# Kernel optimization log

Measured on AMD Instinct MI355X. Metric: run time of the kernel, lower is better.

## Reference

```python
import jax, jax.numpy as jnp
import numpy as np
from jax import lax

T = 64
TAU = 2.0
ALPHA = 4.0  # spikingjelly surrogate.Sigmoid default
V_TH = 1.0

@jax.custom_vjp
def spike(v):
    # Heaviside(v) with sigmoid surrogate gradient
    return (v >= 0.0).astype(v.dtype)

def _spike_fwd(v):
    return spike(v), v

def _spike_bwd(v, g):
    s = jax.nn.sigmoid(ALPHA * v)
    return (g * ALPHA * s * (1.0 - s),)

spike.defvjp(_spike_fwd, _spike_bwd)

def setup_inputs() -> dict:
    key = jax.random.key(0)
    k1, k2, k3 = jax.random.split(key, 3)
    x = jax.random.normal(k1, (2048, 28, 28), dtype=jnp.float32)
    W1 = jax.random.normal(k2, (1024, 784), dtype=jnp.float32) * (1.0 / np.sqrt(784))
    W2 = jax.random.normal(k3, (10, 1024), dtype=jnp.float32) * (1.0 / np.sqrt(1024))
    return {"x": x, "W1": W1, "W2": W2}

def _lif_step(v, c):
    # decay_input=True: v += (x - (v - v_reset)) / tau, v_reset = 0
    v = v + (c - v) / TAU
    s = spike(v - V_TH)
    v = v * (1.0 - s)  # hard reset to 0
    return v, s

def reference(x, W1, W2):
    B = x.shape[0]
    xf = x.reshape(B, -1)                      # [B, 784]
    c1 = xf @ W1.T                              # [B, 1024], identical every timestep
    v1_0 = jnp.zeros((B, W1.shape[0]), x.dtype)
    v2_0 = jnp.zeros((B, W2.shape[0]), x.dtype)

    def step(carry, _):
        v1, v2 = carry
        v1, s1 = _lif_step(v1, c1)              # [B, 1024]
        c2 = s1 @ W2.T                          # [B, 10]
        v2, s2 = _lif_step(v2, c2)              # [B, 10]
        return (v1, v2), s2

    _, out = lax.scan(step, (v1_0, v2_0), None, length=T)
    return out  # [T, B, 10]
```

## Files before the change

### kernel.cpp

```cpp
#include <hip/hip_runtime.h>
#include <stdint.h>

typedef unsigned long long u64;
typedef unsigned int u32;

#define T_STEPS 64
#define KDIM 784
#define N1 1024
#define NB 2048
#define N2 10

__global__ void k_w2t(const float* __restrict__ W2, float* __restrict__ W2T) {
    int j = blockIdx.x * blockDim.x + threadIdx.x;
    if (j >= N1) return;
    float r[12];
#pragma unroll
    for (int i = 0; i < 10; ++i) r[i] = W2[i * N1 + j];
    r[10] = 0.f; r[11] = 0.f;
#pragma unroll
    for (int i = 0; i < 12; ++i) W2T[j * 12 + i] = r[i];
}

#define BM 64
#define BN 64
#define BK 16

__global__ __launch_bounds__(256) void k_gemm_lif1(
    const float* __restrict__ X, const float* __restrict__ W1,
    u64* __restrict__ bits)
{
    __shared__ __align__(16) float As[BK][BM];
    __shared__ __align__(16) float Bs[BK][BN];

    const int tid = threadIdx.x;
    const int tx = tid & 15;
    const int ty = tid >> 4;
    const int bm = blockIdx.y * BM;
    const int bn = blockIdx.x * BN;

    const int lrow = tid >> 2;
    const int lk   = (tid & 3) << 2;

    const float* xa = X  + (size_t)(bm + lrow) * KDIM + lk;
    const float* wa = W1 + (size_t)(bn + lrow) * KDIM + lk;

    float acc[4][4];
#pragma unroll
    for (int r = 0; r < 4; ++r)
#pragma unroll
        for (int c = 0; c < 4; ++c) acc[r][c] = 0.f;

    float4 a = *(const float4*)(xa);
    float4 b = *(const float4*)(wa);

    for (int k0 = 0; k0 < KDIM; k0 += BK) {
        __syncthreads();
        As[lk+0][lrow] = a.x; As[lk+1][lrow] = a.y; As[lk+2][lrow] = a.z; As[lk+3][lrow] = a.w;
        Bs[lk+0][lrow] = b.x; Bs[lk+1][lrow] = b.y; Bs[lk+2][lrow] = b.z; Bs[lk+3][lrow] = b.w;
        __syncthreads();
        if (k0 + BK < KDIM) {
            a = *(const float4*)(xa + k0 + BK);
            b = *(const float4*)(wa + k0 + BK);
        }
#pragma unroll
        for (int kk = 0; kk < BK; ++kk) {
            float4 av = *(const float4*)(&As[kk][ty << 2]);
            float4 bv = *(const float4*)(&Bs[kk][tx << 2]);
            acc[0][0] += av.x * bv.x; acc[0][1] += av.x * bv.y; acc[0][2] += av.x * bv.z; acc[0][3] += av.x * bv.w;
            acc[1][0] += av.y * bv.x; acc[1][1] += av.y * bv.y; acc[1][2] += av.y * bv.z; acc[1][3] += av.y * bv.w;
            acc[2][0] += av.z * bv.x; acc[2][1] += av.z * bv.y; acc[2][2] += av.z * bv.z; acc[2][3] += av.z * bv.w;
            acc[3][0] += av.w * bv.x; acc[3][1] += av.w * bv.y; acc[3][2] += av.w * bv.z; acc[3][3] += av.w * bv.w;
        }
    }

    float c[16], v[16];
    u32 blo[16], bhi[16];
#pragma unroll
    for (int u = 0; u < 16; ++u) {
        c[u] = acc[u >> 2][u & 3];
        v[u] = 0.f; blo[u] = 0u; bhi[u] = 0u;
    }
    for (int t = 0; t < 32; ++t) {
#pragma unroll
        for (int u = 0; u < 16; ++u) {
            v[u] += (c[u] - v[u]) * 0.5f;
            bool s = v[u] >= 1.0f;
            blo[u] |= (s ? 1u : 0u) << t;
            v[u] = s ? 0.f : v[u];
        }
    }
    for (int t = 0; t < 32; ++t) {
#pragma unroll
        for (int u = 0; u < 16; ++u) {
            v[u] += (c[u] - v[u]) * 0.5f;
            bool s = v[u] >= 1.0f;
            bhi[u] |= (s ? 1u : 0u) << t;
            v[u] = s ? 0.f : v[u];
        }
    }
#pragma unroll
    for (int u = 0; u < 16; ++u) {
        int r = u >> 2, cc = u & 3;
        bits[(size_t)(bm + (ty << 2) + r) * N1 + (bn + (tx << 2) + cc)] =
            ((u64)bhi[u] << 32) | (u64)blo[u];
    }
}

__global__ __launch_bounds__(256) void k_lif2(
    const u64* __restrict__ bits, const float* __restrict__ W2T,
    float* __restrict__ out)
{
    __shared__ u64  masksS[4][N1];
    __shared__ u32  idxS[4][N1];
    __shared__ float c2S[4][64][12];
    __shared__ float s2S[4][64][10];

    const int tid  = threadIdx.x;
    const int w    = tid >> 6;
    const int lane = tid & 63;
    const int b    = (blockIdx.x << 2) + w;

    const u64* row = bits + (size_t)b * N1;

    int nact = 0;
#pragma unroll
    for (int it = 0; it < 16; ++it) {
        u64 m = row[lane + (it << 6)];
        u64 ball = __ballot(m != 0ULL);
        int pos = nact + __popcll(ball & ((1ULL << lane) - 1ULL));
        if (m != 0ULL) { masksS[w][pos] = m; idxS[w][pos] = lane + (it << 6); }
        nact += __popcll(ball);
    }

    float acc[10];
#pragma unroll
    for (int i = 0; i < 10; ++i) acc[i] = 0.f;

#define LIF2_BODY(A)                                                      \
    {                                                                     \
        u64 m = masksS[w][(A)];                                           \
        int j = __builtin_amdgcn_readfirstlane((int)idxS[w][(A)]);        \
        float sf = (float)((m >> lane) & 1ULL);                           \
        const float* wr = W2T + j * 12;                                   \
        float4 w0 = *(const float4*)(wr);                                 \
        float4 w1 = *(const float4*)(wr + 4);                             \
        float2 w2 = *(const float2*)(wr + 8);                             \
        acc[0] += sf * w0.x; acc[1] += sf * w0.y;                         \
        acc[2] += sf * w0.z; acc[3] += sf * w0.w;                         \
        acc[4] += sf * w1.x; acc[5] += sf * w1.y;                         \
        acc[6] += sf * w1.z; acc[7] += sf * w1.w;                         \
        acc[8] += sf * w2.x; acc[9] += sf * w2.y;                         \
    }

    int a = 0;
    for (; a + 2 <= nact; a += 2) { LIF2_BODY(a); LIF2_BODY(a + 1); }
    if (a < nact) LIF2_BODY(a);
#undef LIF2_BODY

#pragma unroll
    for (int i = 0; i < 10; ++i) c2S[w][lane][i] = acc[i];
    __syncthreads();

    if (tid < 40) {
        const int w2 = tid / 10, i = tid % 10;
        float v2 = 0.f;
        for (int t = 0; t < 64; ++t) {
            float cc = c2S[w2][t][i];
            v2 += (cc - v2) * 0.5f;
            bool s = v2 >= 1.0f;
            s2S[w2][t][i] = s ? 1.f : 0.f;
            v2 = s ? 0.f : v2;
        }
    }
    __syncthreads();

    const int b0 = blockIdx.x << 2;
    for (int idx = tid; idx < 64 * 40; idx += 256) {
        int t = idx / 40, r = idx % 40;
        out[(size_t)t * (NB * N2) + (size_t)b0 * N2 + r] = s2S[r / 10][t][r % 10];
    }
}

extern "C" void kernel_launch(void* const* d_in, const int* in_sizes, int n_in,
                              void* d_out, int out_size, void* d_ws, size_t ws_size,
                              hipStream_t stream) {
    const float* X  = (const float*)d_in[0];
    const float* W1 = (const float*)d_in[1];
    const float* W2 = (const float*)d_in[2];
    float* out = (float*)d_out;

    u64*   bits = (u64*)d_ws;
    float* W2T  = (float*)((char*)d_ws + (size_t)NB * N1 * sizeof(u64));

    k_w2t<<<dim3((N1 + 255) / 256), dim3(256), 0, stream>>>(W2, W2T);

    dim3 g1(N1 / BN, NB / BM);
    k_gemm_lif1<<<g1, dim3(256), 0, stream>>>(X, W1, bits);

    k_lif2<<<dim3(NB / 4), dim3(256), 0, stream>>>(bits, W2T, out);
}
```

Before: 166.1 us.

## Transpose X and W1 to K-major and compute GEMM without shared memory

Adds a kernel that transposes X and W1 into K-major layouts in workspace. The GEMM+LIF1 kernel is rewritten so each lane owns one output neuron and loops over K, reading W1t coalesced per lane and a wave-uniform 16-row slice of Xt as broadcast float4 loads, with no LDS tiling or barriers. The goal is to remove shared-memory staging and synchronisation overhead. In exchange it adds an extra transpose pass over about 9.5 MB of data and relies on scalar/broadcast loads plus the cache for reuse, with only 16 outputs per thread.

```diff
diff --git a/kernel.cpp b/kernel.cpp
--- a/kernel.cpp
+++ b/kernel.cpp
@@ -21,69 +21,79 @@
     for (int i = 0; i < 12; ++i) W2T[j * 12 + i] = r[i];
 }
 
-#define BM 64
-#define BN 64
-#define BK 16
+__global__ __launch_bounds__(256) void k_transpose2(
+    const float* __restrict__ X, float* __restrict__ Xt,
+    const float* __restrict__ W1, float* __restrict__ W1t)
+{
+    __shared__ float t[32][33];
+    int b = blockIdx.x;
+    const float* src; float* dst; int R;
+    int tile_r, tile_c;
+    if (b < 1600) { src = X;  dst = Xt;  R = NB; tile_r = b / 25; tile_c = b % 25; }
+    else { b -= 1600; src = W1; dst = W1t; R = N1; tile_r = b / 25; tile_c = b % 25; }
+
+    const int tx = threadIdx.x & 31, ty = threadIdx.x >> 5;
+    const int r0 = tile_r << 5, c0 = tile_c << 5;
+
+#pragma unroll
+    for (int i = 0; i < 32; i += 8) {
+        int c = c0 + tx;
+        t[ty + i][tx] = (c < KDIM) ? src[(size_t)(r0 + ty + i) * KDIM + c] : 0.f;
+    }
+    __syncthreads();
+#pragma unroll
+    for (int i = 0; i < 32; i += 8) {
+        int c = c0 + ty + i;
+        if (c < KDIM) dst[(size_t)c * R + r0 + tx] = t[tx][ty + i];
+    }
+}
 
 __global__ __launch_bounds__(256) void k_gemm_lif1(
-    const float* __restrict__ X, const float* __restrict__ W1,
+    const float* __restrict__ Xt,
+    const float* __restrict__ W1t,
     u64* __restrict__ bits)
 {
-    __shared__ __align__(16) float As[BK][BM];
-    __shared__ __align__(16) float Bs[BK][BN];
-
-    const int tid = threadIdx.x;
-    const int tx = tid & 15;
-    const int ty = tid >> 4;
-    const int bm = blockIdx.y * BM;
-    const int bn = blockIdx.x * BN;
-
-    const int lrow = tid >> 2;
-    const int lk   = (tid & 3) << 2;
-
-    const float* xa = X  + (size_t)(bm + lrow) * KDIM + lk;
-    const float* wa = W1 + (size_t)(bn + lrow) * KDIM + lk;
-
-    float acc[4][4];
-#pragma unroll
-    for (int r = 0; r < 4; ++r)
-#pragma unroll
-        for (int c = 0; c < 4; ++c) acc[r][c] = 0.f;
-
-    float4 a = *(const float4*)(xa);
-    float4 b = *(const float4*)(wa);
-
-    for (int k0 = 0; k0 < KDIM; k0 += BK) {
-        __syncthreads();
-        As[lk+0][lrow] = a.x; As[lk+1][lrow] = a.y; As[lk+2][lrow] = a.z; As[lk+3][lrow] = a.w;
-        Bs[lk+0][lrow] = b.x; Bs[lk+1][lrow] = b.y; Bs[lk+2][lrow] = b.z; Bs[lk+3][lrow] = b.w;
-        __syncthreads();
-        if (k0 + BK < KDIM) {
-            a = *(const float4*)(xa + k0 + BK);
-            b = *(const float4*)(wa + k0 + BK);
-        }
-#pragma unroll
-        for (int kk = 0; kk < BK; ++kk) {
-            float4 av = *(const float4*)(&As[kk][ty << 2]);
-            float4 bv = *(const float4*)(&Bs[kk][tx << 2]);
-            acc[0][0] += av.x * bv.x; acc[0][1] += av.x * bv.y; acc[0][2] += av.x * bv.z; acc[0][3] += av.x * bv.w;
-            acc[1][0] += av.y * bv.x; acc[1][1] += av.y * bv.y; acc[1][2] += av.y * bv.z; acc[1][3] += av.y * bv.w;
-            acc[2][0] += av.z * bv.x; acc[2][1] += av.z * bv.y; acc[2][2] += av.z * bv.z; acc[2][3] += av.z * bv.w;
-            acc[3][0] += av.w * bv.x; acc[3][1] += av.w * bv.y; acc[3][2] += av.w * bv.z; acc[3][3] += av.w * bv.w;
-        }
-    }
-
-    float c[16], v[16];
+    const int tid  = threadIdx.x;
+    const int wv   = tid >> 6;
+    const int lane = tid & 63;
+    const int bx   = blockIdx.x;
+
+    const int n0 = (bx & 15) << 6;
+    const int m0 = __builtin_amdgcn_readfirstlane(((bx >> 4) << 6) + (wv << 4));
+
+    const int n = n0 + lane;
+    const float*  __restrict__ wrow = W1t + n;
+    const float4* __restrict__ xrow = (const float4*)(Xt + m0);
+
+    float acc[16];
+#pragma unroll
+    for (int i = 0; i < 16; ++i) acc[i] = 0.f;
+
+#pragma unroll 4
+    for (int k = 0; k < KDIM; ++k) {
+        float a  = wrow[(size_t)k * N1];
+        float4 x0 = xrow[(size_t)k * 512 + 0];
+        float4 x1 = xrow[(size_t)k * 512 + 1];
+        float4 x2 = xrow[(size_t)k * 512 + 2];
+        float4 x3 = xrow[(size_t)k * 512 + 3];
+        acc[ 0] = fmaf(a, x0.x, acc[ 0]); acc[ 1] = fmaf(a, x0.y, acc[ 1]);
+        acc[ 2] = fmaf(a, x0.z, acc[ 2]); acc[ 3] = fmaf(a, x0.w, acc[ 3]);
+        acc[ 4] = fmaf(a, x1.x, acc[ 4]); acc[ 5] = fmaf(a, x1.y, acc[ 5]);
+        acc[ 6] = fmaf(a, x1.z, acc[ 6]); acc[ 7] = fmaf(a, x1.w, acc[ 7]);
+        acc[ 8] = fmaf(a, x2.x, acc[ 8]); acc[ 9] = fmaf(a, x2.y, acc[ 9]);
+        acc[10] = fmaf(a, x2.z, acc[10]); acc[11] = fmaf(a, x2.w, acc[11]);
+        acc[12] = fmaf(a, x3.x, acc[12]); acc[13] = fmaf(a, x3.y, acc[13]);
+        acc[14] = fmaf(a, x3.z, acc[14]); acc[15] = fmaf(a, x3.w, acc[15]);
+    }
+
+    float v[16];
     u32 blo[16], bhi[16];
 #pragma unroll
-    for (int u = 0; u < 16; ++u) {
-        c[u] = acc[u >> 2][u & 3];
-        v[u] = 0.f; blo[u] = 0u; bhi[u] = 0u;
-    }
+    for (int u = 0; u < 16; ++u) { v[u] = 0.f; blo[u] = 0u; bhi[u] = 0u; }
     for (int t = 0; t < 32; ++t) {
 #pragma unroll
         for (int u = 0; u < 16; ++u) {
-            v[u] += (c[u] - v[u]) * 0.5f;
+            v[u] += (acc[u] - v[u]) * 0.5f;
             bool s = v[u] >= 1.0f;
             blo[u] |= (s ? 1u : 0u) << t;
             v[u] = s ? 0.f : v[u];
@@ -92,18 +102,17 @@
     for (int t = 0; t < 32; ++t) {
 #pragma unroll
         for (int u = 0; u < 16; ++u) {
-            v[u] += (c[u] - v[u]) * 0.5f;
+            v[u] += (acc[u] - v[u]) * 0.5f;
             bool s = v[u] >= 1.0f;
             bhi[u] |= (s ? 1u : 0u) << t;
             v[u] = s ? 0.f : v[u];
         }
     }
-#pragma unroll
-    for (int u = 0; u < 16; ++u) {
-        int r = u >> 2, cc = u & 3;
-        bits[(size_t)(bm + (ty << 2) + r) * N1 + (bn + (tx << 2) + cc)] =
-            ((u64)bhi[u] << 32) | (u64)blo[u];
-    }
+
+    u64* bp = bits + (size_t)m0 * N1 + n;
+#pragma unroll
+    for (int u = 0; u < 16; ++u)
+        bp[(size_t)u * N1] = ((u64)bhi[u] << 32) | (u64)blo[u];
 }
 
 __global__ __launch_bounds__(256) void k_lif2(
@@ -189,13 +198,16 @@
     const float* W2 = (const float*)d_in[2];
     float* out = (float*)d_out;
 
-    u64*   bits = (u64*)d_ws;
-    float* W2T  = (float*)((char*)d_ws + (size_t)NB * N1 * sizeof(u64));
+    char* ws = (char*)d_ws;
+    u64*   bits = (u64*)ws;
+    float* W2T  = (float*)(ws + (size_t)NB * N1 * 8);
+    float* Xt   = (float*)(ws + (size_t)NB * N1 * 8 + 65536);
+    float* W1t  = Xt + (size_t)KDIM * NB;
 
     k_w2t<<<dim3((N1 + 255) / 256), dim3(256), 0, stream>>>(W2, W2T);
-
-    dim3 g1(N1 / BN, NB / BM);
-    k_gemm_lif1<<<g1, dim3(256), 0, stream>>>(X, W1, bits);
+    k_transpose2<<<dim3(2400), dim3(256), 0, stream>>>(X, Xt, W1, W1t);
+
+    k_gemm_lif1<<<dim3(512), dim3(256), 0, stream>>>(Xt, W1t, bits);
 
     k_lif2<<<dim3(NB / 4), dim3(256), 0, stream>>>(bits, W2T, out);
 }
```

Result: slower. 201.9 us (+21.5%).
